# Kernel tuning notes

Hardware: AMD Instinct MI355X
Metric: run time of the kernel (lower is better)

## Reference

```python
import jax, jax.numpy as jnp
import numpy as np
import math

B, T, D = 4, 8192, 512
E, K, F = 8, 2, 2048
CAP_FACTOR = 1.25


def setup_inputs() -> dict:
    key = jax.random.key(0)
    ks = jax.random.split(key, 4)
    return {
        "x": jax.random.normal(ks[0], (B, T, D), jnp.float32),
        "gate_w": jax.random.normal(ks[1], (E, D), jnp.float32) * 0.01,  # std=0.01 init
        "w1": jax.random.normal(ks[2], (E, D, F), jnp.float32) * (1.0 / np.sqrt(D)),
        "b1": jnp.zeros((E, F), jnp.float32),
        "w2": jax.random.normal(ks[3], (E, F, D), jnp.float32) * (1.0 / np.sqrt(F)),
        "b2": jnp.zeros((E, D), jnp.float32),
    }


def reference(x, gate_w, w1, b1, w2, b2):
    Bx, Tx, Dx = x.shape
    N = Bx * Tx
    C = math.ceil(CAP_FACTOR * N / E)  # per-expert capacity
    xf = x.reshape(N, Dx)

    # --- Router (eval mode: no noise) ---
    probs = jax.nn.softmax(xf @ gate_w.T, axis=-1)            # (N, E)
    topk_vals, topk_idx = jax.lax.top_k(probs, K)             # (N, K)
    topk_vals = topk_vals / topk_vals.sum(-1, keepdims=True)

    # --- Capacity-based dispatch: token-major, k-minor assignment order,
    #     matching the original serial double loop exactly. ---
    flat_e = topk_idx.reshape(N * K)                          # (NK,)
    onehot = jax.nn.one_hot(flat_e, E, dtype=jnp.int32)       # (NK, E)
    # slot within expert = number of earlier assignments to same expert
    pos = jnp.cumsum(onehot, axis=0)[jnp.arange(N * K), flat_e] - 1
    keep = pos < C                                            # tokens over capacity are dropped
    pos_safe = jnp.where(keep, pos, C)                        # route drops to pad slot C
    token_ids = jnp.repeat(jnp.arange(N), K)

    # --- Gather tokens into (E, C, D) expert buffers (slot C is trash) ---
    buf = jnp.zeros((E, C + 1, Dx), x.dtype).at[flat_e, pos_safe].set(xf[token_ids])
    expert_in = buf[:, :C]                                    # (E, C, D)

    # --- Per-expert FFN (exact GELU, dropout=0 in eval) ---
    h = jax.nn.gelu(jnp.einsum('ecd,edf->ecf', expert_in, w1) + b1[:, None, :],
                    approximate=False)                        # (E, C, F)
    expert_out = jnp.einsum('ecf,efd->ecd', h, w2) + b2[:, None, :]  # (E, C, D)

    # --- Weighted combine back to tokens ---
    gathered = expert_out[flat_e, jnp.minimum(pos_safe, C - 1)]      # (NK, D)
    w = (topk_vals.reshape(N * K) * keep).astype(x.dtype)            # zero for dropped
    out = (gathered * w[:, None]).reshape(N, K, Dx).sum(axis=1)      # (N, D)
    return out.reshape(Bx, Tx, Dx)
```

## Files before the change

### kernel.cpp

```cpp
#include <hip/hip_runtime.h>
#include <math.h>

#define Bx 4
#define Tt 8192
#define Nn (Bx * Tt)
#define Dd 512
#define Ee 8
#define Kk 2
#define Ff 2048
#define Cc 5120
#define NK (Nn * Kk)

typedef unsigned short ushort_t;
typedef __attribute__((ext_vector_type(8))) short bf16x8;
typedef __attribute__((ext_vector_type(4))) float f32x4;

__device__ __forceinline__ float gelu_exact(float v) {
    return 0.5f * v * (1.0f + erff(v * 0.70710678118654752440f));
}

__device__ __forceinline__ ushort_t f2bf(float f) {
    union { float f; unsigned u; } v; v.f = f;
    unsigned r = v.u + 0x7fffu + ((v.u >> 16) & 1u);
    return (ushort_t)(r >> 16);
}

__device__ __forceinline__ void gload_lds16(const ushort_t* g, short* l) {
    __builtin_amdgcn_global_load_lds(
        (const __attribute__((address_space(1))) unsigned int*)g,
        (__attribute__((address_space(3))) unsigned int*)l, 16, 0, 0);
}

__device__ __forceinline__ void swz_decode(int gx, int gy, int& x, int& y, int& z) {
    int nwg = gridDim.x * gridDim.y * gridDim.z;
    int orig = blockIdx.x + gridDim.x * (blockIdx.y + gridDim.y * blockIdx.z);
    int cpx = nwg >> 3;
    int id = (orig & 7) * cpx + (orig >> 3);
    x = id % gx; id /= gx;
    y = id % gy; z = id / gy;
}

__global__ __launch_bounds__(256) void moe_gate_kernel(
    const float* __restrict__ x, const float* __restrict__ gate_w,
    int* __restrict__ flat_e, float* __restrict__ wArr) {
    __shared__ float gw[Ee * Dd];
    int tid = threadIdx.x;
    for (int i = tid; i < 1024; i += 256)
        ((float4*)gw)[i] = ((const float4*)gate_w)[i];
    __syncthreads();

    int wave = tid >> 6, lane = tid & 63;
    int token = blockIdx.x * 4 + wave;

    const float4* xr = (const float4*)(x + (size_t)token * Dd);
    float4 xa = xr[lane];
    float4 xb = xr[lane + 64];

    float acc[Ee];
#pragma unroll
    for (int e = 0; e < Ee; e++) {
        const float4* g = (const float4*)(gw + e * Dd);
        float4 ga = g[lane], gb = g[lane + 64];
        acc[e] = xa.x * ga.x + xa.y * ga.y + xa.z * ga.z + xa.w * ga.w +
                 xb.x * gb.x + xb.y * gb.y + xb.z * gb.z + xb.w * gb.w;
    }
#pragma unroll
    for (int off = 32; off >= 1; off >>= 1) {
#pragma unroll
        for (int e = 0; e < Ee; e++) acc[e] += __shfl_xor(acc[e], off, 64);
    }

    if (lane == 0) {
        float m = acc[0];
#pragma unroll
        for (int e = 1; e < Ee; e++) m = fmaxf(m, acc[e]);
        float p[Ee], s = 0.f;
#pragma unroll
        for (int e = 0; e < Ee; e++) { p[e] = expf(acc[e] - m); s += p[e]; }
        int i0 = 0;
#pragma unroll
        for (int e = 1; e < Ee; e++) if (p[e] > p[i0]) i0 = e;
        int i1 = (i0 == 0) ? 1 : 0;
#pragma unroll
        for (int e = 0; e < Ee; e++) if (e != i0 && p[e] > p[i1]) i1 = e;
        float v0 = p[i0] / s, v1 = p[i1] / s;
        float inv = 1.f / (v0 + v1);
        flat_e[token * 2 + 0] = i0;
        flat_e[token * 2 + 1] = i1;
        wArr[token * 2 + 0] = v0 * inv;
        wArr[token * 2 + 1] = v1 * inv;
    }
}

__global__ __launch_bounds__(256) void moe_hist_kernel(
    const int* __restrict__ flat_e, int* __restrict__ blockCounts) {
    __shared__ int cnt[Ee];
    int tid = threadIdx.x;
    if (tid < Ee) cnt[tid] = 0;
    __syncthreads();
    int e = flat_e[blockIdx.x * 256 + tid];
    atomicAdd(&cnt[e], 1);
    __syncthreads();
    if (tid < Ee) blockCounts[blockIdx.x * Ee + tid] = cnt[tid];
}

__global__ void moe_scan_kernel(const int* __restrict__ blockCounts,
                                int* __restrict__ blockOffsets,
                                int* __restrict__ counts) {
    int e = threadIdx.x;
    if (e >= Ee) return;
    int run = 0;
    for (int b = 0; b < 256; b++) {
        blockOffsets[b * Ee + e] = run;
        run += blockCounts[b * Ee + e];
    }
    counts[e] = min(run, Cc);
}

__global__ __launch_bounds__(256) void moe_scatter_kernel(
    const int* __restrict__ flat_e, const float* __restrict__ wArr,
    const int* __restrict__ blockOffsets,
    int* __restrict__ srcOf, float* __restrict__ wSlot) {
    __shared__ int waveCnt[4][Ee];
    int tid = threadIdx.x;
    int i = blockIdx.x * 256 + tid;
    int e = flat_e[i];
    int wv = tid >> 6, lane = tid & 63;
    unsigned long long ltmask = (1ull << lane) - 1ull;
    int myrank = 0;
#pragma unroll
    for (int ee = 0; ee < Ee; ee++) {
        unsigned long long m = __ballot(e == ee);
        if (e == ee) myrank = __popcll(m & ltmask);
        if (lane == 0) waveCnt[wv][ee] = __popcll(m);
    }
    __syncthreads();
    int base = blockOffsets[blockIdx.x * Ee + e];
    for (int w = 0; w < wv; w++) base += waveCnt[w][e];
    int pos = base + myrank;
    if (pos < Cc) {
        srcOf[e * Cc + pos] = i >> 1;
        wSlot[e * Cc + pos] = wArr[i];
    }
}

__global__ __launch_bounds__(256) void moe_transpose_kernel(
    const float* __restrict__ in, ushort_t* __restrict__ out, int R, int Cn) {
    __shared__ float t[32][33];
    int ez = blockIdx.z;
    const float* ine = in + (size_t)ez * R * Cn;
    ushort_t* oute = out + (size_t)ez * R * Cn;
    int tx = threadIdx.x & 31, ty = threadIdx.x >> 5;
    int r0 = blockIdx.y * 32, c0 = blockIdx.x * 32;
#pragma unroll
    for (int j = 0; j < 4; j++)
        t[ty + j * 8][tx] = ine[(size_t)(r0 + ty + j * 8) * Cn + c0 + tx];
    __syncthreads();
#pragma unroll
    for (int j = 0; j < 4; j++)
        oute[(size_t)(c0 + ty + j * 8) * R + r0 + tx] = f2bf(t[tx][ty + j * 8]);
}

__global__ __launch_bounds__(256) void moe_gather_kernel(
    const float* __restrict__ x, const int* __restrict__ srcOf,
    const int* __restrict__ counts, int chunk0, ushort_t* __restrict__ xg) {
    int tid = threadIdx.x, wave = tid >> 6, lane = tid & 63;
    int sl = blockIdx.x * 4 + wave;
    int le = sl / Cc, c = sl - le * Cc;
    int e = chunk0 + le;
    int cnt = counts[e];
    ushort_t* dst = xg + (size_t)sl * Dd + lane * 8;
    uint4 o;
    if (c < cnt) {
        int src = srcOf[e * Cc + c];
        const float4* xr = (const float4*)(x + (size_t)src * Dd + lane * 8);
        float4 v0 = xr[0], v1 = xr[1];
        o.x = (unsigned)f2bf(v0.x) | ((unsigned)f2bf(v0.y) << 16);
        o.y = (unsigned)f2bf(v0.z) | ((unsigned)f2bf(v0.w) << 16);
        o.z = (unsigned)f2bf(v1.x) | ((unsigned)f2bf(v1.y) << 16);
        o.w = (unsigned)f2bf(v1.z) | ((unsigned)f2bf(v1.w) << 16);
    } else {
        o = make_uint4(0, 0, 0, 0);
    }
    *(uint4*)dst = o;
}


#define GSTAGE(gA, gB, Al, Bl, buf, t, wbase)                                  \
    do {                                                                       \
        int _k = (t) * 32;                                                     \
        gload_lds16((gA) + _k,      &(Al)[(buf) * 4096 + (wbase)]);            \
        gload_lds16((gA) + _k + 16, &(Al)[(buf) * 4096 + 2048 + (wbase)]);     \
        gload_lds16((gB) + _k,      &(Bl)[(buf) * 4096 + (wbase)]);            \
        gload_lds16((gB) + _k + 16, &(Bl)[(buf) * 4096 + 2048 + (wbase)]);     \
    } while (0)

__global__ __launch_bounds__(256) void moe_mfma_gemm1(
    const ushort_t* __restrict__ xg, const ushort_t* __restrict__ w1t,
    const float* __restrict__ b1, int chunk0, ushort_t* __restrict__ hbuf) {
    int bx, by, le;
    swz_decode(Ff / 128, Cc / 128, bx, by, le);
    int e = chunk0 + le;
    const ushort_t* A = xg + (size_t)le * Cc * Dd;
    const ushort_t* Bt = w1t + (size_t)e * Ff * Dd;
    const float* bias = b1 + (size_t)e * Ff;
    ushort_t* h = hbuf + (size_t)le * Cc * Ff;

    __shared__ short Al[2 * 4096];
    __shared__ short Bl[2 * 4096];

    int tid = threadIdx.x;
    int lane = tid & 63, wave = tid >> 6;
    int wr = wave >> 1, wc = wave & 1;
    int m0 = by * 128;
    int n0 = bx * 128;
    int kslot = lane >> 4, lr = lane & 15;
    int aoff = (kslot * 128 + wr * 64 + lr) * 8;
    int boff = (kslot * 128 + wc * 64 + lr) * 8;
    int wbase = (tid & 192) * 8;
    int row = tid & 127, ks0 = tid >> 7;

    const ushort_t* gA = A + (size_t)(m0 + row) * Dd + ks0 * 8;
    const ushort_t* gB = Bt + (size_t)(n0 + row) * Dd + ks0 * 8;

    f32x4 acc[4][4] = {};
    const int NT = Dd / 32;

    GSTAGE(gA, gB, Al, Bl, 0, 0, wbase);
    for (int t = 0; t < NT; ++t) {
        int cur = t & 1;
        if (t + 1 < NT) {
            GSTAGE(gA, gB, Al, Bl, cur ^ 1, t + 1, wbase);
            asm volatile("s_waitcnt vmcnt(4)" ::: "memory");
        } else {
            asm volatile("s_waitcnt vmcnt(0)" ::: "memory");
        }
        __builtin_amdgcn_s_barrier();
        asm volatile("" ::: "memory");
        bf16x8 a[4], b[4];
        int ab = cur * 4096 + aoff, bb = cur * 4096 + boff;
#pragma unroll
        for (int m = 0; m < 4; ++m) a[m] = *(const bf16x8*)&Al[ab + m * 128];
#pragma unroll
        for (int n = 0; n < 4; ++n) b[n] = *(const bf16x8*)&Bl[bb + n * 128];
#pragma unroll
        for (int m = 0; m < 4; ++m)
#pragma unroll
            for (int n = 0; n < 4; ++n)
                acc[m][n] = __builtin_amdgcn_mfma_f32_16x16x32_bf16(
                    a[m], b[n], acc[m][n], 0, 0, 0);
        asm volatile("" ::: "memory");
        __builtin_amdgcn_s_barrier();
    }

    float bv[4];
#pragma unroll
    for (int n = 0; n < 4; ++n) bv[n] = bias[n0 + wc * 64 + n * 16 + lr];
#pragma unroll
    for (int m = 0; m < 4; ++m) {
#pragma unroll
        for (int r = 0; r < 4; ++r) {
            int orow = m0 + wr * 64 + m * 16 + kslot * 4 + r;
            size_t base = (size_t)orow * Ff + n0 + wc * 64 + lr;
#pragma unroll
            for (int n = 0; n < 4; ++n)
                h[base + n * 16] = f2bf(gelu_exact(acc[m][n][r] + bv[n]));
        }
    }
}

__global__ __launch_bounds__(256) void moe_mfma_gemm2(
    const ushort_t* __restrict__ hbuf, const ushort_t* __restrict__ w2t,
    const float* __restrict__ b2, const int* __restrict__ srcOf,
    const float* __restrict__ wSlot, const int* __restrict__ counts,
    int chunk0, float* __restrict__ out) {
    int bx, by, le;
    swz_decode(Dd / 128, Cc / 128, bx, by, le);
    int e = chunk0 + le;
    const ushort_t* A = hbuf + (size_t)le * Cc * Ff;
    const ushort_t* Bt = w2t + (size_t)e * Dd * Ff;
    const float* bias = b2 + (size_t)e * Dd;
    const int* srcE = srcOf + (size_t)e * Cc;
    const float* wE = wSlot + (size_t)e * Cc;
    int count = counts[e];

    __shared__ short Al[2 * 4096];
    __shared__ short Bl[2 * 4096];

    int tid = threadIdx.x;
    int lane = tid & 63, wave = tid >> 6;
    int wr = wave >> 1, wc = wave & 1;
    int m0 = by * 128;
    int n0 = bx * 128;
    int kslot = lane >> 4, lr = lane & 15;
    int aoff = (kslot * 128 + wr * 64 + lr) * 8;
    int boff = (kslot * 128 + wc * 64 + lr) * 8;
    int wbase = (tid & 192) * 8;
    int row = tid & 127, ks0 = tid >> 7;

    const ushort_t* gA = A + (size_t)(m0 + row) * Ff + ks0 * 8;
    const ushort_t* gB = Bt + (size_t)(n0 + row) * Ff + ks0 * 8;

    f32x4 acc[4][4] = {};
    const int NT = Ff / 32;

    GSTAGE(gA, gB, Al, Bl, 0, 0, wbase);
    for (int t = 0; t < NT; ++t) {
        int cur = t & 1;
        if (t + 1 < NT) {
            GSTAGE(gA, gB, Al, Bl, cur ^ 1, t + 1, wbase);
            asm volatile("s_waitcnt vmcnt(4)" ::: "memory");
        } else {
            asm volatile("s_waitcnt vmcnt(0)" ::: "memory");
        }
        __builtin_amdgcn_s_barrier();
        asm volatile("" ::: "memory");
        bf16x8 a[4], b[4];
        int ab = cur * 4096 + aoff, bb = cur * 4096 + boff;
#pragma unroll
        for (int m = 0; m < 4; ++m) a[m] = *(const bf16x8*)&Al[ab + m * 128];
#pragma unroll
        for (int n = 0; n < 4; ++n) b[n] = *(const bf16x8*)&Bl[bb + n * 128];
#pragma unroll
        for (int m = 0; m < 4; ++m)
#pragma unroll
            for (int n = 0; n < 4; ++n)
                acc[m][n] = __builtin_amdgcn_mfma_f32_16x16x32_bf16(
                    a[m], b[n], acc[m][n], 0, 0, 0);
        asm volatile("" ::: "memory");
        __builtin_amdgcn_s_barrier();
    }

    float bv[4];
#pragma unroll
    for (int n = 0; n < 4; ++n) bv[n] = bias[n0 + wc * 64 + n * 16 + lr];
#pragma unroll
    for (int m = 0; m < 4; ++m) {
#pragma unroll
        for (int r = 0; r < 4; ++r) {
            int orow = m0 + wr * 64 + m * 16 + kslot * 4 + r;
            if (orow < count) {
                int token = srcE[orow];
                float wgt = wE[orow];
                float* op = out + (size_t)token * Dd + n0 + wc * 64 + lr;
#pragma unroll
                for (int n = 0; n < 4; ++n)
                    atomicAdd(&op[n * 16], wgt * (acc[m][n][r] + bv[n]));
            }
        }
    }
}

extern "C" void kernel_launch(void* const* d_in, const int* in_sizes, int n_in,
                              void* d_out, int out_size, void* d_ws, size_t ws_size,
                              hipStream_t stream) {
    const float* x      = (const float*)d_in[0];
    const float* gate_w = (const float*)d_in[1];
    const float* w1     = (const float*)d_in[2];
    const float* b1     = (const float*)d_in[3];
    const float* w2     = (const float*)d_in[4];
    const float* b2     = (const float*)d_in[5];
    float* out = (float*)d_out;

    char* p = (char*)d_ws;
    int*      flat_e       = (int*)p;       p += (size_t)NK * 4;
    float*    wArr         = (float*)p;     p += (size_t)NK * 4;
    int*      blockCounts  = (int*)p;       p += 256 * Ee * 4;
    int*      blockOffsets = (int*)p;       p += 256 * Ee * 4;
    int*      counts       = (int*)p;       p += 64 * 4;
    int*      srcOf        = (int*)p;       p += (size_t)Ee * Cc * 4;
    float*    wSlot        = (float*)p;     p += (size_t)Ee * Cc * 4;
    p = (char*)(((size_t)p + 255) & ~(size_t)255);
    ushort_t* w1t          = (ushort_t*)p;  p += (size_t)Ee * Dd * Ff * 2;
    ushort_t* w2t          = (ushort_t*)p;  p += (size_t)Ee * Ff * Dd * 2;
    size_t fixedEnd = (size_t)(p - (char*)d_ws);
    size_t avail = (ws_size > fixedEnd) ? ws_size - fixedEnd : 0;

    size_t perE = (size_t)Cc * Dd * 2 + (size_t)Cc * Ff * 2;
    int P = Ee;
    while (P > 1 && (size_t)P * perE > avail) P >>= 1;
    ushort_t* xg = (ushort_t*)((char*)d_ws + fixedEnd);
    ushort_t* hbuf = xg + (size_t)P * Cc * Dd;

    moe_gate_kernel<<<Nn / 4, 256, 0, stream>>>(x, gate_w, flat_e, wArr);
    moe_hist_kernel<<<NK / 256, 256, 0, stream>>>(flat_e, blockCounts);
    moe_scan_kernel<<<1, 64, 0, stream>>>(blockCounts, blockOffsets, counts);
    moe_scatter_kernel<<<NK / 256, 256, 0, stream>>>(flat_e, wArr, blockOffsets,
                                                     srcOf, wSlot);
    moe_transpose_kernel<<<dim3(Ff / 32, Dd / 32, Ee), 256, 0, stream>>>(
        w1, w1t, Dd, Ff);
    moe_transpose_kernel<<<dim3(Dd / 32, Ff / 32, Ee), 256, 0, stream>>>(
        w2, w2t, Ff, Dd);
    hipMemsetAsync(d_out, 0, (size_t)Nn * Dd * sizeof(float), stream);

    for (int c0 = 0; c0 < Ee; c0 += P) {
        moe_gather_kernel<<<P * Cc / 4, 256, 0, stream>>>(x, srcOf, counts, c0, xg);
        moe_mfma_gemm1<<<dim3(Ff / 128, Cc / 128, P), 256, 0, stream>>>(
            xg, w1t, b1, c0, hbuf);
        moe_mfma_gemm2<<<dim3(Dd / 128, Cc / 128, P), 256, 0, stream>>>(
            hbuf, w2t, b2, srcOf, wSlot, counts, c0, out);
    }
}
```

Measured before the change: 653.3 us.

## Enlarge MFMA GEMM tiles to 256-row blocks with 512 threads and split prefetch

Both expert GEMMs now use 512-thread blocks with larger output tiles (256x256 for the first GEMM, 256x128 for the second) and a K-step of 64 split into two halves. The prefetch of the next K-tile is issued in two parts, interleaved between the two MFMA half-steps, and MFMA sections raise wave priority with s_setprio. The aim is more data reuse per global load and better overlap of loads with compute. In exchange it uses more LDS and registers per block (acc[8][4] in GEMM1), which may reduce occupancy, and leaves fewer blocks to spread over the CUs.

```diff
diff --git a/kernel.cpp b/kernel.cpp
--- a/kernel.cpp
+++ b/kernel.cpp
@@ -186,82 +186,113 @@
 }
 
 
-#define GSTAGE(gA, gB, Al, Bl, buf, t, wbase)                                  \
-    do {                                                                       \
-        int _k = (t) * 32;                                                     \
-        gload_lds16((gA) + _k,      &(Al)[(buf) * 4096 + (wbase)]);            \
-        gload_lds16((gA) + _k + 16, &(Al)[(buf) * 4096 + 2048 + (wbase)]);     \
-        gload_lds16((gB) + _k,      &(Bl)[(buf) * 4096 + (wbase)]);            \
-        gload_lds16((gB) + _k + 16, &(Bl)[(buf) * 4096 + 2048 + (wbase)]);     \
-    } while (0)
-
-__global__ __launch_bounds__(256) void moe_mfma_gemm1(
+__global__ __launch_bounds__(512, 2) void moe_mfma_gemm1(
     const ushort_t* __restrict__ xg, const ushort_t* __restrict__ w1t,
     const float* __restrict__ b1, int chunk0, ushort_t* __restrict__ hbuf) {
     int bx, by, le;
-    swz_decode(Ff / 128, Cc / 128, bx, by, le);
+    swz_decode(Ff / 256, Cc / 256, bx, by, le);
     int e = chunk0 + le;
     const ushort_t* A = xg + (size_t)le * Cc * Dd;
     const ushort_t* Bt = w1t + (size_t)e * Ff * Dd;
     const float* bias = b1 + (size_t)e * Ff;
     ushort_t* h = hbuf + (size_t)le * Cc * Ff;
 
-    __shared__ short Al[2 * 4096];
-    __shared__ short Bl[2 * 4096];
+    __shared__ short Al[2 * 16384];
+    __shared__ short Bl[2 * 16384];
 
     int tid = threadIdx.x;
     int lane = tid & 63, wave = tid >> 6;
-    int wr = wave >> 1, wc = wave & 1;
-    int m0 = by * 128;
-    int n0 = bx * 128;
+    int wr = wave >> 2, wn = wave & 3;
+    int m0 = by * 256, n0 = bx * 256;
     int kslot = lane >> 4, lr = lane & 15;
-    int aoff = (kslot * 128 + wr * 64 + lr) * 8;
-    int boff = (kslot * 128 + wc * 64 + lr) * 8;
-    int wbase = (tid & 192) * 8;
-    int row = tid & 127, ks0 = tid >> 7;
-
-    const ushort_t* gA = A + (size_t)(m0 + row) * Dd + ks0 * 8;
-    const ushort_t* gB = Bt + (size_t)(n0 + row) * Dd + ks0 * 8;
-
-    f32x4 acc[4][4] = {};
-    const int NT = Dd / 32;
-
-    GSTAGE(gA, gB, Al, Bl, 0, 0, wbase);
+    int wvofs = (tid & 0x1C0) * 8;
+
+    const ushort_t* pA[4];
+    const ushort_t* pB[4];
+#pragma unroll
+    for (int c = 0; c < 4; ++c) {
+        int idx = c * 512 + tid;
+        pA[c] = A + (size_t)(m0 + (idx & 255)) * Dd + (idx >> 8) * 8;
+        pB[c] = Bt + (size_t)(n0 + (idx & 255)) * Dd + (idx >> 8) * 8;
+    }
+
+    f32x4 acc[8][4] = {};
+    const int NT = Dd / 64;
+
+#pragma unroll
+    for (int c = 0; c < 4; ++c) gload_lds16(pA[c], &Al[c * 4096 + wvofs]);
+#pragma unroll
+    for (int c = 0; c < 4; ++c) gload_lds16(pB[c], &Bl[c * 4096 + wvofs]);
+
     for (int t = 0; t < NT; ++t) {
-        int cur = t & 1;
+        int cur = t & 1, nb = (cur ^ 1) * 16384;
+        int kn = (t + 1) * 64;
         if (t + 1 < NT) {
-            GSTAGE(gA, gB, Al, Bl, cur ^ 1, t + 1, wbase);
+            gload_lds16(pA[0] + kn, &Al[nb + 0 * 4096 + wvofs]);
+            gload_lds16(pA[1] + kn, &Al[nb + 1 * 4096 + wvofs]);
+            gload_lds16(pB[0] + kn, &Bl[nb + 0 * 4096 + wvofs]);
+            gload_lds16(pB[1] + kn, &Bl[nb + 1 * 4096 + wvofs]);
             asm volatile("s_waitcnt vmcnt(4)" ::: "memory");
         } else {
             asm volatile("s_waitcnt vmcnt(0)" ::: "memory");
         }
         __builtin_amdgcn_s_barrier();
         asm volatile("" ::: "memory");
-        bf16x8 a[4], b[4];
-        int ab = cur * 4096 + aoff, bb = cur * 4096 + boff;
-#pragma unroll
-        for (int m = 0; m < 4; ++m) a[m] = *(const bf16x8*)&Al[ab + m * 128];
-#pragma unroll
-        for (int n = 0; n < 4; ++n) b[n] = *(const bf16x8*)&Bl[bb + n * 128];
-#pragma unroll
-        for (int m = 0; m < 4; ++m)
+        {
+            bf16x8 a[8], b[4];
+            int ab = cur * 16384;
+#pragma unroll
+            for (int m = 0; m < 8; ++m)
+                a[m] = *(const bf16x8*)&Al[ab + (kslot * 256 + wr * 128 + m * 16 + lr) * 8];
 #pragma unroll
             for (int n = 0; n < 4; ++n)
-                acc[m][n] = __builtin_amdgcn_mfma_f32_16x16x32_bf16(
-                    a[m], b[n], acc[m][n], 0, 0, 0);
+                b[n] = *(const bf16x8*)&Bl[ab + (kslot * 256 + wn * 64 + n * 16 + lr) * 8];
+            __builtin_amdgcn_s_setprio(1);
+#pragma unroll
+            for (int m = 0; m < 8; ++m)
+#pragma unroll
+                for (int n = 0; n < 4; ++n)
+                    acc[m][n] = __builtin_amdgcn_mfma_f32_16x16x32_bf16(
+                        a[m], b[n], acc[m][n], 0, 0, 0);
+            __builtin_amdgcn_s_setprio(0);
+        }
+        if (t + 1 < NT) {
+            gload_lds16(pA[2] + kn, &Al[nb + 2 * 4096 + wvofs]);
+            gload_lds16(pA[3] + kn, &Al[nb + 3 * 4096 + wvofs]);
+            gload_lds16(pB[2] + kn, &Bl[nb + 2 * 4096 + wvofs]);
+            gload_lds16(pB[3] + kn, &Bl[nb + 3 * 4096 + wvofs]);
+        }
+        {
+            bf16x8 a[8], b[4];
+            int ab = cur * 16384 + 8192;
+#pragma unroll
+            for (int m = 0; m < 8; ++m)
+                a[m] = *(const bf16x8*)&Al[ab + (kslot * 256 + wr * 128 + m * 16 + lr) * 8];
+#pragma unroll
+            for (int n = 0; n < 4; ++n)
+                b[n] = *(const bf16x8*)&Bl[ab + (kslot * 256 + wn * 64 + n * 16 + lr) * 8];
+            __builtin_amdgcn_s_setprio(1);
+#pragma unroll
+            for (int m = 0; m < 8; ++m)
+#pragma unroll
+                for (int n = 0; n < 4; ++n)
+                    acc[m][n] = __builtin_amdgcn_mfma_f32_16x16x32_bf16(
+                        a[m], b[n], acc[m][n], 0, 0, 0);
+            __builtin_amdgcn_s_setprio(0);
+        }
         asm volatile("" ::: "memory");
         __builtin_amdgcn_s_barrier();
     }
 
     float bv[4];
 #pragma unroll
-    for (int n = 0; n < 4; ++n) bv[n] = bias[n0 + wc * 64 + n * 16 + lr];
-#pragma unroll
-    for (int m = 0; m < 4; ++m) {
+    for (int n = 0; n < 4; ++n) bv[n] = bias[n0 + wn * 64 + n * 16 + lr];
+#pragma unroll
+    for (int m = 0; m < 8; ++m) {
 #pragma unroll
         for (int r = 0; r < 4; ++r) {
-            int orow = m0 + wr * 64 + m * 16 + kslot * 4 + r;
-            size_t base = (size_t)orow * Ff + n0 + wc * 64 + lr;
+            int orow = m0 + wr * 128 + m * 16 + kslot * 4 + r;
+            size_t base = (size_t)orow * Ff + n0 + wn * 64 + lr;
 #pragma unroll
             for (int n = 0; n < 4; ++n)
                 h[base + n * 16] = f2bf(gelu_exact(acc[m][n][r] + bv[n]));
@@ -269,13 +300,13 @@
     }
 }
 
-__global__ __launch_bounds__(256) void moe_mfma_gemm2(
+__global__ __launch_bounds__(512, 2) void moe_mfma_gemm2(
     const ushort_t* __restrict__ hbuf, const ushort_t* __restrict__ w2t,
     const float* __restrict__ b2, const int* __restrict__ srcOf,
     const float* __restrict__ wSlot, const int* __restrict__ counts,
     int chunk0, float* __restrict__ out) {
     int bx, by, le;
-    swz_decode(Dd / 128, Cc / 128, bx, by, le);
+    swz_decode(Dd / 128, Cc / 256, bx, by, le);
     int e = chunk0 + le;
     const ushort_t* A = hbuf + (size_t)le * Cc * Ff;
     const ushort_t* Bt = w2t + (size_t)e * Dd * Ff;
@@ -284,56 +315,100 @@
     const float* wE = wSlot + (size_t)e * Cc;
     int count = counts[e];
 
-    __shared__ short Al[2 * 4096];
-    __shared__ short Bl[2 * 4096];
+    __shared__ short Al[2 * 16384];
+    __shared__ short Bl[2 * 8192];
 
     int tid = threadIdx.x;
     int lane = tid & 63, wave = tid >> 6;
-    int wr = wave >> 1, wc = wave & 1;
-    int m0 = by * 128;
-    int n0 = bx * 128;
+    int wr = wave >> 1, wn = wave & 1;
+    int m0 = by * 256, n0 = bx * 128;
     int kslot = lane >> 4, lr = lane & 15;
-    int aoff = (kslot * 128 + wr * 64 + lr) * 8;
-    int boff = (kslot * 128 + wc * 64 + lr) * 8;
-    int wbase = (tid & 192) * 8;
-    int row = tid & 127, ks0 = tid >> 7;
-
-    const ushort_t* gA = A + (size_t)(m0 + row) * Ff + ks0 * 8;
-    const ushort_t* gB = Bt + (size_t)(n0 + row) * Ff + ks0 * 8;
+    int wvofs = (tid & 0x1C0) * 8;
+
+    const ushort_t* pA[4];
+    const ushort_t* pB[2];
+#pragma unroll
+    for (int c = 0; c < 4; ++c) {
+        int idx = c * 512 + tid;
+        pA[c] = A + (size_t)(m0 + (idx & 255)) * Ff + (idx >> 8) * 8;
+    }
+#pragma unroll
+    for (int c = 0; c < 2; ++c) {
+        int idx = c * 512 + tid;
+        pB[c] = Bt + (size_t)(n0 + (idx & 127)) * Ff + (idx >> 7) * 8;
+    }
 
     f32x4 acc[4][4] = {};
-    const int NT = Ff / 32;
-
-    GSTAGE(gA, gB, Al, Bl, 0, 0, wbase);
+    const int NT = Ff / 64;
+
+#pragma unroll
+    for (int c = 0; c < 4; ++c) gload_lds16(pA[c], &Al[c * 4096 + wvofs]);
+#pragma unroll
+    for (int c = 0; c < 2; ++c) gload_lds16(pB[c], &Bl[c * 4096 + wvofs]);
+
     for (int t = 0; t < NT; ++t) {
         int cur = t & 1;
+        int nbA = (cur ^ 1) * 16384, nbB = (cur ^ 1) * 8192;
+        int kn = (t + 1) * 64;
         if (t + 1 < NT) {
-            GSTAGE(gA, gB, Al, Bl, cur ^ 1, t + 1, wbase);
-            asm volatile("s_waitcnt vmcnt(4)" ::: "memory");
+            gload_lds16(pA[0] + kn, &Al[nbA + 0 * 4096 + wvofs]);
+            gload_lds16(pA[1] + kn, &Al[nbA + 1 * 4096 + wvofs]);
+            gload_lds16(pB[0] + kn, &Bl[nbB + 0 * 4096 + wvofs]);
+            asm volatile("s_waitcnt vmcnt(3)" ::: "memory");
         } else {
             asm volatile("s_waitcnt vmcnt(0)" ::: "memory");
         }
         __builtin_amdgcn_s_barrier();
         asm volatile("" ::: "memory");
-        bf16x8 a[4], b[4];
-        int ab = cur * 4096 + aoff, bb = cur * 4096 + boff;
-#pragma unroll
-        for (int m = 0; m < 4; ++m) a[m] = *(const bf16x8*)&Al[ab + m * 128];
-#pragma unroll
-        for (int n = 0; n < 4; ++n) b[n] = *(const bf16x8*)&Bl[bb + n * 128];
-#pragma unroll
-        for (int m = 0; m < 4; ++m)
+        {
+            bf16x8 a[4], b[4];
+            int ab = cur * 16384, bb = cur * 8192;
+#pragma unroll
+            for (int m = 0; m < 4; ++m)
+                a[m] = *(const bf16x8*)&Al[ab + (kslot * 256 + wr * 64 + m * 16 + lr) * 8];
 #pragma unroll
             for (int n = 0; n < 4; ++n)
-                acc[m][n] = __builtin_amdgcn_mfma_f32_16x16x32_bf16(
-                    a[m], b[n], acc[m][n], 0, 0, 0);
+                b[n] = *(const bf16x8*)&Bl[bb + (kslot * 128 + wn * 64 + n * 16 + lr) * 8];
+            __builtin_amdgcn_s_setprio(1);
+#pragma unroll
+            for (int m = 0; m < 4; ++m)
+#pragma unroll
+                for (int n = 0; n < 4; ++n)
+                    acc[m][n] = __builtin_amdgcn_mfma_f32_16x16x32_bf16(
+                        a[m], b[n], acc[m][n], 0, 0, 0);
+            __builtin_amdgcn_s_setprio(0);
+        }
+        if (t + 1 < NT) {
+            gload_lds16(pA[2] + kn, &Al[nbA + 2 * 4096 + wvofs]);
+            gload_lds16(pA[3] + kn, &Al[nbA + 3 * 4096 + wvofs]);
+            gload_lds16(pB[1] + kn, &Bl[nbB + 1 * 4096 + wvofs]);
+        }
+        {
+            bf16x8 a[4], b[4];
+            int ab = cur * 16384 + 8192;
+            int bb = cur * 8192 + 4096;
+#pragma unroll
+            for (int m = 0; m < 4; ++m)
+                a[m] = *(const bf16x8*)&Al[ab + (kslot * 256 + wr * 64 + m * 16 + lr) * 8];
+#pragma unroll
+            for (int n = 0; n < 4; ++n)
+                b[n] = *(const bf16x8*)&Bl[bb + (kslot * 128 + wn * 64 + n * 16 + lr) * 8];
+            __builtin_amdgcn_s_setprio(1);
+#pragma unroll
+            for (int m = 0; m < 4; ++m)
+#pragma unroll
+                for (int n = 0; n < 4; ++n)
+                    acc[m][n] = __builtin_amdgcn_mfma_f32_16x16x32_bf16(
+                        a[m], b[n], acc[m][n], 0, 0, 0);
+            __builtin_amdgcn_s_setprio(0);
+        }
         asm volatile("" ::: "memory");
         __builtin_amdgcn_s_barrier();
     }
 
     float bv[4];
 #pragma unroll
-    for (int n = 0; n < 4; ++n) bv[n] = bias[n0 + wc * 64 + n * 16 + lr];
+    for (int n = 0; n < 4; ++n) bv[n] = bias[n0 + wn * 64 + n * 16 + lr];
 #pragma unroll
     for (int m = 0; m < 4; ++m) {
 #pragma unroll
@@ -342,7 +417,7 @@
             if (orow < count) {
                 int token = srcE[orow];
                 float wgt = wE[orow];
-                float* op = out + (size_t)token * Dd + n0 + wc * 64 + lr;
+                float* op = out + (size_t)token * Dd + n0 + wn * 64 + lr;
 #pragma unroll
                 for (int n = 0; n < 4; ++n)
                     atomicAdd(&op[n * 16], wgt * (acc[m][n][r] + bv[n]));
@@ -395,9 +470,9 @@
 
     for (int c0 = 0; c0 < Ee; c0 += P) {
         moe_gather_kernel<<<P * Cc / 4, 256, 0, stream>>>(x, srcOf, counts, c0, xg);
-        moe_mfma_gemm1<<<dim3(Ff / 128, Cc / 128, P), 256, 0, stream>>>(
+        moe_mfma_gemm1<<<dim3(Ff / 256, Cc / 256, P), 512, 0, stream>>>(
             xg, w1t, b1, c0, hbuf);
-        moe_mfma_gemm2<<<dim3(Dd / 128, Cc / 128, P), 256, 0, stream>>>(
+        moe_mfma_gemm2<<<dim3(Dd / 128, Cc / 256, P), 512, 0, stream>>>(
             hbuf, w2t, b2, srcOf, wSlot, counts, c0, out);
     }
 }
```

Result: slower. 690.7 us (+5.7%).
